# Optimization experiments

Measured on AMD Instinct MI355X. Metric: run time of the kernel, lower is better.

Reference implementation:

```python
import jax, jax.numpy as jnp
import numpy as np

N = 50000
E = 800000
F_IN = 64
F_OUT = 64


def setup_inputs() -> dict:
    key = jax.random.key(0)
    ks = jax.random.split(key, 14)
    x = jax.random.normal(ks[0], (N, F_IN), dtype=jnp.float32)
    row_low = jax.random.randint(ks[1], (E,), 0, N)
    col_low = jax.random.randint(ks[2], (E,), 0, N)
    val_low = jax.random.uniform(ks[3], (E,), dtype=jnp.float32)
    row_high = jax.random.randint(ks[4], (E,), 0, N)
    col_high = jax.random.randint(ks[5], (E,), 0, N)
    val_high = jax.random.uniform(ks[6], (E,), dtype=jnp.float32)
    # xavier-uniform style init for weights
    def xavier(k, shape):
        fan_in, fan_out = shape[0], shape[1]
        bound = float(np.sqrt(6.0 / (fan_in + fan_out)))
        return jax.random.uniform(k, shape, jnp.float32, -bound, bound)
    W_low = xavier(ks[7], (F_IN, F_OUT))
    W_high = xavier(ks[8], (F_IN, F_OUT))
    W_mlp = xavier(ks[9], (F_IN, F_OUT))
    a_low = xavier(ks[10], (F_OUT, 1))
    a_high = xavier(ks[11], (F_OUT, 1))
    a_mlp = xavier(ks[12], (F_OUT, 1))
    att3 = xavier(ks[13], (3, 3))
    return dict(x=x, row_low=row_low, col_low=col_low, val_low=val_low,
                row_high=row_high, col_high=col_high, val_high=val_high,
                W_low=W_low, W_high=W_high, W_mlp=W_mlp,
                a_low=a_low, a_high=a_high, a_mlp=a_mlp, att3=att3)


def _spmm(row, col, val, h, n):
    # (sparse adj) @ h : gather source rows, scale by edge weight, scatter-add to dest
    return jax.ops.segment_sum(val[:, None] * h[col], row, num_segments=n)


def reference(x, row_low, col_low, val_low, row_high, col_high, val_high,
              W_low, W_high, W_mlp, a_low, a_high, a_mlp, att3):
    n = x.shape[0]
    out_low = jax.nn.relu(_spmm(row_low, col_low, val_low, x @ W_low, n))
    out_high = jax.nn.relu(_spmm(row_high, col_high, val_high, x @ W_high, n))
    out_mlp = jax.nn.relu(x @ W_mlp)
    T = 3.0
    feats = jnp.concatenate([out_low @ a_low, out_high @ a_high, out_mlp @ a_mlp], axis=1)  # [N,3]
    logits = (jax.nn.sigmoid(feats) @ att3) / T
    att = jax.nn.softmax(logits, axis=1)  # [N,3]
    return 3.0 * (att[:, 0:1] * out_low + att[:, 1:2] * out_high + att[:, 2:3] * out_mlp)
```

## Files before the change

kernel.cpp:

```cpp
#include <hip/hip_runtime.h>


#define NNODE 50000
#define NEDGE 800000
#define NBUCK 782
#define CAP   1552

typedef __attribute__((ext_vector_type(8))) short short8v;
typedef __attribute__((ext_vector_type(4))) float float4v;

__device__ __forceinline__ unsigned short f2bf(float f) {
    unsigned u = __float_as_uint(f);
    u += 0x7FFFu + ((u >> 16) & 1u);
    return (unsigned short)(u >> 16);
}

__global__ __launch_bounds__(256)
void zero_kernel(unsigned int* __restrict__ g)
{
    const int i = blockIdx.x * 256 + threadIdx.x;
    if (i < 2 * NBUCK) g[i] = 0u;
}

__global__ __launch_bounds__(256)
void gemm_mfma_kernel(const float* __restrict__ x,
                      const float* __restrict__ Wl, const float* __restrict__ Wh,
                      const float* __restrict__ Wm,
                      unsigned short* __restrict__ hl16,
                      unsigned short* __restrict__ hh16,
                      unsigned short* __restrict__ hm16)
{
    __shared__ unsigned short wt[3][64][72];
    const int t = threadIdx.x;
#pragma unroll 1
    for (int m = 0; m < 3; ++m) {
        const float* __restrict__ W = (m == 0) ? Wl : (m == 1) ? Wh : Wm;
        for (int i = t; i < 4096; i += 256) {
            const int k = i >> 6, c = i & 63;
            wt[m][c][k] = f2bf(W[i]);
        }
    }
    __syncthreads();

    const int wid = t >> 6, lane = t & 63;
    const int node0 = blockIdx.x * 64 + wid * 16;
    if (node0 >= NNODE) return;
    const int arow = lane & 15;
    const int hi = lane >> 4;

    const float* __restrict__ xr = x + (size_t)(node0 + arow) * 64 + hi * 8;
    const float4 pa0 = *(const float4*)(xr + 0);
    const float4 pa1 = *(const float4*)(xr + 4);
    const float4 pb0 = *(const float4*)(xr + 32);
    const float4 pb1 = *(const float4*)(xr + 36);
    short8v a0, a1;
    a0[0] = (short)f2bf(pa0.x); a0[1] = (short)f2bf(pa0.y);
    a0[2] = (short)f2bf(pa0.z); a0[3] = (short)f2bf(pa0.w);
    a0[4] = (short)f2bf(pa1.x); a0[5] = (short)f2bf(pa1.y);
    a0[6] = (short)f2bf(pa1.z); a0[7] = (short)f2bf(pa1.w);
    a1[0] = (short)f2bf(pb0.x); a1[1] = (short)f2bf(pb0.y);
    a1[2] = (short)f2bf(pb0.z); a1[3] = (short)f2bf(pb0.w);
    a1[4] = (short)f2bf(pb1.x); a1[5] = (short)f2bf(pb1.y);
    a1[6] = (short)f2bf(pb1.z); a1[7] = (short)f2bf(pb1.w);

#pragma unroll 1
    for (int m = 0; m < 3; ++m) {
        unsigned short* __restrict__ H = (m == 0) ? hl16 : (m == 1) ? hh16 : hm16;
        float4v acc0 = {0.f, 0.f, 0.f, 0.f}, acc1 = {0.f, 0.f, 0.f, 0.f};
        float4v acc2 = {0.f, 0.f, 0.f, 0.f}, acc3 = {0.f, 0.f, 0.f, 0.f};

#define DO_CT(CT, ACC)                                                          \
        {                                                                       \
            const short8v b0 = *(const short8v*)&wt[m][CT * 16 + arow][hi * 8]; \
            const short8v b1 = *(const short8v*)&wt[m][CT * 16 + arow][32 + hi * 8]; \
            ACC = __builtin_amdgcn_mfma_f32_16x16x32_bf16(a0, b0, ACC, 0, 0, 0); \
            ACC = __builtin_amdgcn_mfma_f32_16x16x32_bf16(a1, b1, ACC, 0, 0, 0); \
        }
        DO_CT(0, acc0) DO_CT(1, acc1) DO_CT(2, acc2) DO_CT(3, acc3)
#undef DO_CT

        const bool rl = (m == 2);
#define ST_CT(CT, ACC)                                                          \
        {                                                                       \
            _Pragma("unroll")                                                   \
            for (int r = 0; r < 4; ++r) {                                       \
                float v = ACC[r];                                               \
                if (rl) v = fmaxf(v, 0.f);                                      \
                H[(size_t)(node0 + hi * 4 + r) * 64 + CT * 16 + arow] = f2bf(v); \
            }                                                                   \
        }
        ST_CT(0, acc0) ST_CT(1, acc1) ST_CT(2, acc2) ST_CT(3, acc3)
#undef ST_CT
    }
}

__global__ __launch_bounds__(512)
void scatter_kernel(const int* __restrict__ row_low, const int* __restrict__ col_low,
                    const float* __restrict__ val_low,
                    const int* __restrict__ row_high, const int* __restrict__ col_high,
                    const float* __restrict__ val_high,
                    unsigned int* __restrict__ gcursor, uint2* __restrict__ packed)
{
    __shared__ unsigned int hist_s[2 * NBUCK];
    __shared__ unsigned int base_s[2 * NBUCK];
    const int t = threadIdx.x;
    const int ebase = blockIdx.x * 8192;

    for (int i = t; i < 2 * NBUCK; i += 512) hist_s[i] = 0u;
    __syncthreads();

    int rows[16]; unsigned int rank[16];
#pragma unroll
    for (int j = 0; j < 16; ++j) {
        const int e = ebase + j * 512 + t;
        rows[j] = 0; rank[j] = 0u;
        if (e < 2 * NEDGE) {
            const int r = (e < NEDGE) ? row_low[e] : row_high[e - NEDGE];
            const int fb = ((e < NEDGE) ? 0 : NBUCK) + (r >> 6);
            rows[j] = r;
            rank[j] = atomicAdd(&hist_s[fb], 1u);
        }
    }
    __syncthreads();
    for (int i = t; i < 2 * NBUCK; i += 512) {
        const unsigned int c = hist_s[i];
        base_s[i] = c ? atomicAdd(&gcursor[i], c) : 0u;
    }
    __syncthreads();
#pragma unroll
    for (int j = 0; j < 16; ++j) {
        const int e = ebase + j * 512 + t;
        if (e < 2 * NEDGE) {
            const int g = (e >= NEDGE);
            const int ee = e - g * NEDGE;
            const int r = rows[j];
            const int c = g ? col_high[ee] : col_low[ee];
            const float v = g ? val_high[ee] : val_low[ee];
            const int fb = g * NBUCK + (r >> 6);
            const unsigned int pos = base_s[fb] + rank[j];
            if (pos < CAP) {
                uint2 pk;
                pk.x = (unsigned int)c | ((unsigned int)(r & 63) << 16);
                pk.y = __float_as_uint(v);
                packed[(size_t)fb * CAP + pos] = pk;
            }
        }
    }
}

__global__ __launch_bounds__(256)
void sort_kernel(uint2* __restrict__ packed,
                 const unsigned int* __restrict__ gcursor,
                 int* __restrict__ rs, int* __restrict__ rc)
{
    __shared__ uint2 es[CAP];
    __shared__ unsigned int hist[64];
    __shared__ unsigned int offs[64];
    __shared__ unsigned int cur[64];

    const int fb = blockIdx.x;
    const int t = threadIdx.x;
    uint2* __restrict__ seg = packed + (size_t)fb * CAP;
    int cnt = (int)gcursor[fb];
    if (cnt > CAP) cnt = CAP;

    if (t < 64) { hist[t] = 0u; cur[t] = 0u; }
    __syncthreads();

    for (int i = t; i < cnt; i += 256) {
        const uint2 p = seg[i];
        es[i] = p;
        atomicAdd(&hist[(p.x >> 16) & 63u], 1u);
    }
    __syncthreads();

    if (t < 64) {
        const int pv = (int)((hist[t] + 7u) & ~7u);
        int xsc = pv;
#pragma unroll
        for (int d = 1; d < 64; d <<= 1) {
            int y = __shfl_up(xsc, d, 64);
            if (t >= d) xsc += y;
        }
        offs[t] = (unsigned)(xsc - pv);
    }
    __syncthreads();

    for (int i = t; i < cnt; i += 256) {
        const uint2 p = es[i];
        const unsigned r = (p.x >> 16) & 63u;
        const unsigned pos = offs[r] + atomicAdd(&cur[r], 1u);
        if (pos < CAP) seg[pos] = p;
    }
    if (t < 64) {
        const unsigned b = offs[t] + hist[t];
        const unsigned e = offs[t] + ((hist[t] + 7u) & ~7u);
        const uint2 z = {0u, 0u};
        for (unsigned u = b; u < e && u < CAP; ++u) seg[u] = z;
    }

    if (t < 64) {
        const int g = (fb >= NBUCK);
        const int node = ((fb - g * NBUCK) << 6) + t;
        if (node < NNODE) {
            const unsigned P = (hist[t] + 7u) & ~7u;
            const int avail = CAP - (int)offs[t];
            int nq = (int)(P >> 2);
            int nqa = avail > 0 ? ((avail >> 2) & ~1) : 0;
            if (nq > nqa) nq = nqa;
            rs[g * NNODE + node] = fb * CAP + (int)offs[t];
            rc[g * NNODE + node] = nq;
        }
    }
}

#define Q_FMA(U_, V_, AX_, AY_, AZ_, AW_)                                      \
    {                                                                          \
        AX_ = fmaf(V_, __uint_as_float(U_.x << 16), AX_);                      \
        AY_ = fmaf(V_, __uint_as_float(U_.x & 0xFFFF0000u), AY_);              \
        AZ_ = fmaf(V_, __uint_as_float(U_.y << 16), AZ_);                      \
        AW_ = fmaf(V_, __uint_as_float(U_.y & 0xFFFF0000u), AW_);              \
    }

__global__ __launch_bounds__(256, 8)
void spmm_finalize_kernel(const uint2* __restrict__ packed,
                          const int* __restrict__ rs, const int* __restrict__ rc,
                          const unsigned short* __restrict__ hl16,
                          const unsigned short* __restrict__ hh16,
                          const unsigned short* __restrict__ hm16,
                          const float* __restrict__ aL, const float* __restrict__ aH,
                          const float* __restrict__ aM, const float* __restrict__ att3,
                          float* __restrict__ out)
{
    const int wid = threadIdx.x >> 6;
    const int lane = threadIdx.x & 63;
    const int sub = lane >> 4;
    const int f4 = (lane & 15) << 2;
    const unsigned fb2 = (unsigned)(f4 * 2);
    const int node = blockIdx.x * 4 + wid;
    if (node >= NNODE) return;

    const int sL = __builtin_amdgcn_readfirstlane(rs[node]);
    const int nqL = __builtin_amdgcn_readfirstlane(rc[node]);
    const int sH = __builtin_amdgcn_readfirstlane(rs[NNODE + node]);
    const int nqH = __builtin_amdgcn_readfirstlane(rc[NNODE + node]);
    const uint2* __restrict__ segL = packed + sL + sub;
    const uint2* __restrict__ segH = packed + sH + sub;
    const int nqm = (nqL > nqH) ? nqL : nqH;

    float lx = 0.f, ly = 0.f, lz = 0.f, lw = 0.f;
    float hx = 0.f, hy = 0.f, hz = 0.f, hw = 0.f;

#pragma unroll 1
    for (int q = 0; q < nqm; q += 2) {
        const uint2 rL0 = segL[q * 4];
        const uint2 rL1 = segL[q * 4 + 4];
        const uint2 rH0 = segH[q * 4];
        const uint2 rH1 = segH[q * 4 + 4];
        const uint2 uL0 = *(const uint2*)((const char*)hl16 + (size_t)(((rL0.x & 0xFFFFu) << 7) + fb2));
        const uint2 uL1 = *(const uint2*)((const char*)hl16 + (size_t)(((rL1.x & 0xFFFFu) << 7) + fb2));
        const uint2 uH0 = *(const uint2*)((const char*)hh16 + (size_t)(((rH0.x & 0xFFFFu) << 7) + fb2));
        const uint2 uH1 = *(const uint2*)((const char*)hh16 + (size_t)(((rH1.x & 0xFFFFu) << 7) + fb2));
        __builtin_amdgcn_sched_barrier(0);
        const float vL0 = (q     < nqL) ? __uint_as_float(rL0.y) : 0.f;
        const float vL1 = (q + 1 < nqL) ? __uint_as_float(rL1.y) : 0.f;
        const float vH0 = (q     < nqH) ? __uint_as_float(rH0.y) : 0.f;
        const float vH1 = (q + 1 < nqH) ? __uint_as_float(rH1.y) : 0.f;
        Q_FMA(uL0, vL0, lx, ly, lz, lw);
        Q_FMA(uL1, vL1, lx, ly, lz, lw);
        Q_FMA(uH0, vH0, hx, hy, hz, hw);
        Q_FMA(uH1, vH1, hx, hy, hz, hw);
    }

    lx += __shfl_xor(lx, 16, 64); ly += __shfl_xor(ly, 16, 64);
    lz += __shfl_xor(lz, 16, 64); lw += __shfl_xor(lw, 16, 64);
    hx += __shfl_xor(hx, 16, 64); hy += __shfl_xor(hy, 16, 64);
    hz += __shfl_xor(hz, 16, 64); hw += __shfl_xor(hw, 16, 64);
    lx += __shfl_xor(lx, 32, 64); ly += __shfl_xor(ly, 32, 64);
    lz += __shfl_xor(lz, 32, 64); lw += __shfl_xor(lw, 32, 64);
    hx += __shfl_xor(hx, 32, 64); hy += __shfl_xor(hy, 32, 64);
    hz += __shfl_xor(hz, 32, 64); hw += __shfl_xor(hw, 32, 64);

    const float olx = fmaxf(lx, 0.f), oly = fmaxf(ly, 0.f);
    const float olz = fmaxf(lz, 0.f), olw = fmaxf(lw, 0.f);
    const float ohx = fmaxf(hx, 0.f), ohy = fmaxf(hy, 0.f);
    const float ohz = fmaxf(hz, 0.f), ohw = fmaxf(hw, 0.f);

    const uint2 om2 = *(const uint2*)&hm16[(size_t)node * 64 + f4];
    const float omx = __uint_as_float(om2.x << 16);
    const float omy = __uint_as_float(om2.x & 0xFFFF0000u);
    const float omz = __uint_as_float(om2.y << 16);
    const float omw = __uint_as_float(om2.y & 0xFFFF0000u);

    const float4 aL4 = *(const float4*)&aL[f4];
    const float4 aH4 = *(const float4*)&aH[f4];
    const float4 aM4 = *(const float4*)&aM[f4];

    float f0 = olx * aL4.x + oly * aL4.y + olz * aL4.z + olw * aL4.w;
    float f1 = ohx * aH4.x + ohy * aH4.y + ohz * aH4.z + ohw * aH4.w;
    float f2 = omx * aM4.x + omy * aM4.y + omz * aM4.z + omw * aM4.w;
#pragma unroll
    for (int msk = 1; msk < 16; msk <<= 1) {
        f0 += __shfl_xor(f0, msk, 64);
        f1 += __shfl_xor(f1, msk, 64);
        f2 += __shfl_xor(f2, msk, 64);
    }
    const float s0 = 1.f / (1.f + __expf(-f0));
    const float s1 = 1.f / (1.f + __expf(-f1));
    const float s2 = 1.f / (1.f + __expf(-f2));
    const float invT = 1.f / 3.f;
    const float l0g = (s0 * att3[0] + s1 * att3[3] + s2 * att3[6]) * invT;
    const float l1g = (s0 * att3[1] + s1 * att3[4] + s2 * att3[7]) * invT;
    const float l2g = (s0 * att3[2] + s1 * att3[5] + s2 * att3[8]) * invT;
    const float mx = fmaxf(l0g, fmaxf(l1g, l2g));
    const float e0 = __expf(l0g - mx);
    const float e1 = __expf(l1g - mx);
    const float e2 = __expf(l2g - mx);
    const float inv = 1.f / (e0 + e1 + e2);
    const float wl = 3.f * inv * e0, wh = 3.f * inv * e1, wm = 3.f * inv * e2;

    if (lane < 16) {
        float4 o;
        o.x = wl * olx + wh * ohx + wm * omx;
        o.y = wl * oly + wh * ohy + wm * omy;
        o.z = wl * olz + wh * ohz + wm * omz;
        o.w = wl * olw + wh * ohw + wm * omw;
        *(float4*)&out[(size_t)node * 64 + f4] = o;
    }
}

extern "C" void kernel_launch(void* const* d_in, const int* in_sizes, int n_in,
                              void* d_out, int out_size, void* d_ws, size_t ws_size,
                              hipStream_t stream)
{
    const float* x        = (const float*)d_in[0];
    const int*   row_low  = (const int*)  d_in[1];
    const int*   col_low  = (const int*)  d_in[2];
    const float* val_low  = (const float*)d_in[3];
    const int*   row_high = (const int*)  d_in[4];
    const int*   col_high = (const int*)  d_in[5];
    const float* val_high = (const float*)d_in[6];
    const float* W_low    = (const float*)d_in[7];
    const float* W_high   = (const float*)d_in[8];
    const float* W_mlp    = (const float*)d_in[9];
    const float* a_low    = (const float*)d_in[10];
    const float* a_high   = (const float*)d_in[11];
    const float* a_mlp    = (const float*)d_in[12];
    const float* att3     = (const float*)d_in[13];
    float* out = (float*)d_out;

    const size_t NM = (size_t)NNODE * 64;

    unsigned short* hl16    = (unsigned short*)d_ws;
    unsigned short* hh16    = hl16 + NM;
    unsigned short* hm16    = hh16 + NM;
    uint2*          packed  = (uint2*)(hm16 + NM);
    unsigned int*   gcursor = (unsigned int*)(packed + (size_t)2 * NBUCK * CAP);
    int*            rs      = (int*)(gcursor + 2 * NBUCK);
    int*            rc      = rs + 2 * NNODE;

    zero_kernel<<<(2 * NBUCK + 255) / 256, 256, 0, stream>>>(gcursor);

    scatter_kernel<<<(2 * NEDGE + 8191) / 8192, 512, 0, stream>>>(
        row_low, col_low, val_low, row_high, col_high, val_high, gcursor, packed);

    gemm_mfma_kernel<<<(NNODE + 63) / 64, 256, 0, stream>>>(
        x, W_low, W_high, W_mlp, hl16, hh16, hm16);

    sort_kernel<<<2 * NBUCK, 256, 0, stream>>>(packed, gcursor, rs, rc);

    spmm_finalize_kernel<<<(NNODE + 3) / 4, 256, 0, stream>>>(
        packed, rs, rc, hl16, hh16, hm16, a_low, a_high, a_mlp, att3, out);
}
```

Baseline: 97.87 us.

## Switch SpMM features and weights to fp16 with packed half2 FMA and prefetch

The stored projected features change from bf16 to fp16, and edge weights are packed as duplicated fp16 pairs. This lets the SpMM inner loop accumulate with packed __hfma2 instead of scalar fp32 FMAs. The edge-record loads are software-pipelined one iteration ahead, so the next pair is fetched while the current gathers run. Accumulating in fp16 across many edges risks precision loss, and the prefetch reads past the end of each segment.

```diff
diff --git a/kernel.cpp b/kernel.cpp
--- a/kernel.cpp
+++ b/kernel.cpp
@@ -1,4 +1,5 @@
 #include <hip/hip_runtime.h>
+#include <hip/hip_fp16.h>
 
 
 #define NNODE 50000
@@ -13,6 +14,9 @@
     unsigned u = __float_as_uint(f);
     u += 0x7FFFu + ((u >> 16) & 1u);
     return (unsigned short)(u >> 16);
+}
+__device__ __forceinline__ __half2 u_as_h2(unsigned u) {
+    return *reinterpret_cast<__half2*>(&u);
 }
 
 __global__ __launch_bounds__(256)
@@ -86,7 +90,8 @@
             for (int r = 0; r < 4; ++r) {                                       \
                 float v = ACC[r];                                               \
                 if (rl) v = fmaxf(v, 0.f);                                      \
-                H[(size_t)(node0 + hi * 4 + r) * 64 + CT * 16 + arow] = f2bf(v); \
+                H[(size_t)(node0 + hi * 4 + r) * 64 + CT * 16 + arow] =         \
+                    __half_as_ushort(__float2half(v));                          \
             }                                                                   \
         }
         ST_CT(0, acc0) ST_CT(1, acc1) ST_CT(2, acc2) ST_CT(3, acc3)
@@ -139,9 +144,10 @@
             const int fb = g * NBUCK + (r >> 6);
             const unsigned int pos = base_s[fb] + rank[j];
             if (pos < CAP) {
+                const unsigned short hb = __half_as_ushort(__float2half(v));
                 uint2 pk;
                 pk.x = (unsigned int)c | ((unsigned int)(r & 63) << 16);
-                pk.y = __float_as_uint(v);
+                pk.y = (unsigned)hb | ((unsigned)hb << 16);
                 packed[(size_t)fb * CAP + pos] = pk;
             }
         }
@@ -214,14 +220,6 @@
     }
 }
 
-#define Q_FMA(U_, V_, AX_, AY_, AZ_, AW_)                                      \
-    {                                                                          \
-        AX_ = fmaf(V_, __uint_as_float(U_.x << 16), AX_);                      \
-        AY_ = fmaf(V_, __uint_as_float(U_.x & 0xFFFF0000u), AY_);              \
-        AZ_ = fmaf(V_, __uint_as_float(U_.y << 16), AZ_);                      \
-        AW_ = fmaf(V_, __uint_as_float(U_.y & 0xFFFF0000u), AW_);              \
-    }
-
 __global__ __launch_bounds__(256, 8)
 void spmm_finalize_kernel(const uint2* __restrict__ packed,
                           const int* __restrict__ rs, const int* __restrict__ rc,
@@ -248,29 +246,45 @@
     const uint2* __restrict__ segH = packed + sH + sub;
     const int nqm = (nqL > nqH) ? nqL : nqH;
 
-    float lx = 0.f, ly = 0.f, lz = 0.f, lw = 0.f;
-    float hx = 0.f, hy = 0.f, hz = 0.f, hw = 0.f;
+    const __half2 hz2 = u_as_h2(0u);
+    __half2 aL0a = hz2, aL1a = hz2, aL0b = hz2, aL1b = hz2;
+    __half2 aH0a = hz2, aH1a = hz2, aH0b = hz2, aH1b = hz2;
+
+    uint2 cL0 = segL[0], cL1 = segL[4];
+    uint2 cH0 = segH[0], cH1 = segH[4];
 
 #pragma unroll 1
     for (int q = 0; q < nqm; q += 2) {
-        const uint2 rL0 = segL[q * 4];
-        const uint2 rL1 = segL[q * 4 + 4];
-        const uint2 rH0 = segH[q * 4];
-        const uint2 rH1 = segH[q * 4 + 4];
-        const uint2 uL0 = *(const uint2*)((const char*)hl16 + (size_t)(((rL0.x & 0xFFFFu) << 7) + fb2));
-        const uint2 uL1 = *(const uint2*)((const char*)hl16 + (size_t)(((rL1.x & 0xFFFFu) << 7) + fb2));
-        const uint2 uH0 = *(const uint2*)((const char*)hh16 + (size_t)(((rH0.x & 0xFFFFu) << 7) + fb2));
-        const uint2 uH1 = *(const uint2*)((const char*)hh16 + (size_t)(((rH1.x & 0xFFFFu) << 7) + fb2));
+        const uint2 nL0 = segL[q * 4 + 8],  nL1 = segL[q * 4 + 12];
+        const uint2 nH0 = segH[q * 4 + 8],  nH1 = segH[q * 4 + 12];
+        const uint2 uL0 = *(const uint2*)((const char*)hl16 + (size_t)(((cL0.x & 0xFFFFu) << 7) + fb2));
+        const uint2 uL1 = *(const uint2*)((const char*)hl16 + (size_t)(((cL1.x & 0xFFFFu) << 7) + fb2));
+        const uint2 uH0 = *(const uint2*)((const char*)hh16 + (size_t)(((cH0.x & 0xFFFFu) << 7) + fb2));
+        const uint2 uH1 = *(const uint2*)((const char*)hh16 + (size_t)(((cH1.x & 0xFFFFu) << 7) + fb2));
         __builtin_amdgcn_sched_barrier(0);
-        const float vL0 = (q     < nqL) ? __uint_as_float(rL0.y) : 0.f;
-        const float vL1 = (q + 1 < nqL) ? __uint_as_float(rL1.y) : 0.f;
-        const float vH0 = (q     < nqH) ? __uint_as_float(rH0.y) : 0.f;
-        const float vH1 = (q + 1 < nqH) ? __uint_as_float(rH1.y) : 0.f;
-        Q_FMA(uL0, vL0, lx, ly, lz, lw);
-        Q_FMA(uL1, vL1, lx, ly, lz, lw);
-        Q_FMA(uH0, vH0, hx, hy, hz, hw);
-        Q_FMA(uH1, vH1, hx, hy, hz, hw);
-    }
+        const __half2 vL0 = u_as_h2((q     < nqL) ? cL0.y : 0u);
+        const __half2 vL1 = u_as_h2((q + 1 < nqL) ? cL1.y : 0u);
+        const __half2 vH0 = u_as_h2((q     < nqH) ? cH0.y : 0u);
+        const __half2 vH1 = u_as_h2((q + 1 < nqH) ? cH1.y : 0u);
+        aL0a = __hfma2(u_as_h2(uL0.x), vL0, aL0a);
+        aL1a = __hfma2(u_as_h2(uL0.y), vL0, aL1a);
+        aL0b = __hfma2(u_as_h2(uL1.x), vL1, aL0b);
+        aL1b = __hfma2(u_as_h2(uL1.y), vL1, aL1b);
+        aH0a = __hfma2(u_as_h2(uH0.x), vH0, aH0a);
+        aH1a = __hfma2(u_as_h2(uH0.y), vH0, aH1a);
+        aH0b = __hfma2(u_as_h2(uH1.x), vH1, aH0b);
+        aH1b = __hfma2(u_as_h2(uH1.y), vH1, aH1b);
+        cL0 = nL0; cL1 = nL1; cH0 = nH0; cH1 = nH1;
+    }
+
+    float lx = __low2float(aL0a) + __low2float(aL0b);
+    float ly = __high2float(aL0a) + __high2float(aL0b);
+    float lz = __low2float(aL1a) + __low2float(aL1b);
+    float lw = __high2float(aL1a) + __high2float(aL1b);
+    float hx = __low2float(aH0a) + __low2float(aH0b);
+    float hy = __high2float(aH0a) + __high2float(aH0b);
+    float hz = __low2float(aH1a) + __low2float(aH1b);
+    float hw = __high2float(aH1a) + __high2float(aH1b);
 
     lx += __shfl_xor(lx, 16, 64); ly += __shfl_xor(ly, 16, 64);
     lz += __shfl_xor(lz, 16, 64); lw += __shfl_xor(lw, 16, 64);
@@ -287,10 +301,10 @@
     const float ohz = fmaxf(hz, 0.f), ohw = fmaxf(hw, 0.f);
 
     const uint2 om2 = *(const uint2*)&hm16[(size_t)node * 64 + f4];
-    const float omx = __uint_as_float(om2.x << 16);
-    const float omy = __uint_as_float(om2.x & 0xFFFF0000u);
-    const float omz = __uint_as_float(om2.y << 16);
-    const float omw = __uint_as_float(om2.y & 0xFFFF0000u);
+    const float omx = __low2float(u_as_h2(om2.x));
+    const float omy = __high2float(u_as_h2(om2.x));
+    const float omz = __low2float(u_as_h2(om2.y));
+    const float omw = __high2float(u_as_h2(om2.y));
 
     const float4 aL4 = *(const float4*)&aL[f4];
     const float4 aH4 = *(const float4*)&aH[f4];
```

New measurement: 101.4 us. +3.6%, slower.
